# Kernel tuning notes

Measured on AMD Instinct MI355X. Metric: run time of the kernel, lower is better.

The kernel has to match this reference:

```python
import jax, jax.numpy as jnp
import numpy as np
from math import sqrt

CTX_LEN = 24
DK = 92
EMBED_DIM = 36
N_TOKENS = 500
HIDDEN = 152
CONCAT_DIM = 936  # 2*EMBED_DIM + EMBED_DIM*CTX_LEN


def setup_inputs() -> dict:
    key = jax.random.key(0)
    ks = jax.random.split(key, 12)
    u = lambda k, shp, s: jax.random.uniform(k, shp, dtype=jnp.float32) * s
    return {
        "x0": jax.random.normal(ks[0], (EMBED_DIM, CTX_LEN), dtype=jnp.float32),
        "wq1": u(ks[1], (CTX_LEN, DK), 0.05),
        "wk1": u(ks[2], (CTX_LEN, DK), 0.05),
        "wv1": u(ks[3], (CTX_LEN, DK), 0.05),
        "wq2": u(ks[4], (CTX_LEN, DK), 0.05),
        "wk2": u(ks[5], (CTX_LEN, DK), 0.05),
        "wv2": u(ks[6], (CTX_LEN, DK), 0.05),
        "nl0": u(ks[7], (CONCAT_DIM, HIDDEN), 0.05),
        "nl0_bias": u(ks[8], (HIDDEN,), 0.005),
        "nl1": u(ks[9], (HIDDEN, EMBED_DIM), 0.05),
        "ctp": u(ks[10], (EMBED_DIM, N_TOKENS), 0.05),
        "ctp_bias": u(ks[11], (N_TOKENS,), 0.005),
    }


def _self_attn(x, wq, wk, wv):
    # x: (E, C); wq/wk/wv: (C, DK)
    q = x @ wq
    k = x @ wk
    v = x @ wv
    # NOTE: original multiplies by sqrt(dk) (not divide) and softmaxes over dim 0
    scores = jax.nn.softmax((q @ k.T) * sqrt(DK), axis=0)  # (E, E)
    return scores @ v  # (E, DK)


def reference(x0, wq1, wk1, wv1, wq2, wk2, wv2, nl0, nl0_bias, nl1, ctp, ctp_bias):
    t3 = _self_attn(x0, wq1, wk1, wv1).sum(axis=1)   # (E,)
    t13 = _self_attn(x0, wq2, wk2, wv2).sum(axis=1)  # (E,)
    t71 = jnp.concatenate([t3, t13, x0.reshape(-1)])  # (936,)
    t7 = jax.nn.relu(t71 @ nl0) + nl0_bias            # (152,)
    t10 = t7 @ nl1                                    # (E,)
    return t10 @ ctp + ctp_bias                       # (N_TOKENS,)
```

## Files before the change

### kernel.cpp

```cpp
#include <hip/hip_runtime.h>
#include <math.h>

#define CTX 24
#define DKK 92
#define ED 36
#define NTOK 500
#define HID 152

#define NBLK 19
#define COLS 8
#define TOKS 27
#define POISON 0xAAAAAAAAu

typedef float4 f4;

__device__ __forceinline__ float dot4(f4 a, f4 b) {
    return a.x*b.x + a.y*b.y + a.z*b.z + a.w*b.w;
}

struct AttnLds {
    f4    xw4[216];
    f4    W4[144];
    f4    M4[216];
    float S[1296];
    float wvs[24];
    f4    vs24[9];
};

__device__ void attn_wave(int lane, const float* __restrict__ x0,
                          const float* __restrict__ wq, const float* __restrict__ wk,
                          const float* __restrict__ wv,
                          AttnLds& L, float* __restrict__ dst )
{
    const f4* x0g = (const f4*)x0;
    for (int i = lane; i < 216; i += 64) L.xw4[i] = x0g[i];
    if (lane < CTX) {
        const f4* wvr = (const f4*)(wv + lane * DKK);
        f4 s = {0.f, 0.f, 0.f, 0.f};
        #pragma unroll
        for (int c = 0; c < 23; ++c) {
            f4 v = wvr[c];
            s.x += v.x; s.y += v.y; s.z += v.z; s.w += v.w;
        }
        L.wvs[lane] = s.x + s.y + s.z + s.w;
    }
    __threadfence_block();

    {
        const f4* wq4 = (const f4*)wq;
        const f4* wk4 = (const f4*)wk;
        const int a0 = (lane >> 3) * 3, b0 = (lane & 7) * 3;
        float acc[3][3] = {};
        #pragma unroll 4
        for (int dc = 0; dc < 23; ++dc) {
            f4 qa[3], kb[3];
            #pragma unroll
            for (int r = 0; r < 3; ++r) qa[r] = wq4[(a0 + r) * 23 + dc];
            #pragma unroll
            for (int c = 0; c < 3; ++c) kb[c] = wk4[(b0 + c) * 23 + dc];
            #pragma unroll
            for (int r = 0; r < 3; ++r)
                #pragma unroll
                for (int c = 0; c < 3; ++c)
                    acc[r][c] += dot4(qa[r], kb[c]);
        }
        float* Wf = (float*)L.W4;
        #pragma unroll
        for (int r = 0; r < 3; ++r)
            #pragma unroll
            for (int c = 0; c < 3; ++c)
                Wf[(a0 + r) * 24 + b0 + c] = acc[r][c];
    }
    __threadfence_block();

    {
        const float* xf = (const float*)L.xw4;
        for (int t = lane; t < 72; t += 64) {
            const int e0 = (t / 6) * 3, bq = t % 6;
            f4 acc[3] = {};
            #pragma unroll
            for (int a = 0; a < 24; ++a) {
                f4 w = L.W4[a * 6 + bq];
                #pragma unroll
                for (int r = 0; r < 3; ++r) {
                    float x = xf[(e0 + r) * 24 + a];
                    acc[r].x += x * w.x; acc[r].y += x * w.y;
                    acc[r].z += x * w.z; acc[r].w += x * w.w;
                }
            }
            #pragma unroll
            for (int r = 0; r < 3; ++r) L.M4[(e0 + r) * 6 + bq] = acc[r];
        }
    }
    __threadfence_block();

    {
        const float scale = 9.59166304662544f;
        for (int t = lane; t < 108; t += 64) {
            const int e0 = (t / 9) * 3, f0 = (t % 9) * 4;
            float acc[3][4] = {};
            #pragma unroll
            for (int bq = 0; bq < 6; ++bq) {
                f4 m[3], x[4];
                #pragma unroll
                for (int r = 0; r < 3; ++r) m[r] = L.M4[(e0 + r) * 6 + bq];
                #pragma unroll
                for (int c = 0; c < 4; ++c) x[c] = L.xw4[(f0 + c) * 6 + bq];
                #pragma unroll
                for (int r = 0; r < 3; ++r)
                    #pragma unroll
                    for (int c = 0; c < 4; ++c)
                        acc[r][c] += dot4(m[r], x[c]);
            }
            #pragma unroll
            for (int r = 0; r < 3; ++r)
                #pragma unroll
                for (int c = 0; c < 4; ++c)
                    L.S[(e0 + r) * 36 + f0 + c] = acc[r][c] * scale;
        }
    }
    __threadfence_block();

    if (lane < ED) {
        const int f = lane;
        float mx = -1e30f;
        #pragma unroll 4
        for (int e = 0; e < ED; ++e) mx = fmaxf(mx, L.S[e * 36 + f]);
        float sum = 0.f;
        #pragma unroll 4
        for (int e = 0; e < ED; ++e) {
            float p = expf(L.S[e * 36 + f] - mx);
            L.S[e * 36 + f] = p;
            sum += p;
        }
        const float* xf = (const float*)L.xw4;
        float vs = 0.f;
        #pragma unroll
        for (int c = 0; c < CTX; ++c) vs += xf[f * 24 + c] * L.wvs[c];
        ((float*)L.vs24)[f] = vs / sum;
    }
    __threadfence_block();

    if (lane < ED) {
        const int e = lane;
        const f4* Srow = (const f4*)&L.S[e * 36];
        float s = 0.f;
        #pragma unroll
        for (int fq = 0; fq < 9; ++fq) s += dot4(Srow[fq], L.vs24[fq]);
        dst[e] = s;
    }
}

__global__ __launch_bounds__(256) void fused_vpoll(
    const float* __restrict__ x0,
    const float* __restrict__ wq1, const float* __restrict__ wk1, const float* __restrict__ wv1,
    const float* __restrict__ wq2, const float* __restrict__ wk2, const float* __restrict__ wv2,
    const float* __restrict__ nl0, const float* __restrict__ nl0_bias,
    const float* __restrict__ nl1, const float* __restrict__ ctp, const float* __restrict__ ctp_bias,
    float* __restrict__ ws, float* __restrict__ out)
{
    __shared__ AttnLds A0, A1;
    __shared__ float conc72[72];
    __shared__ f4    part4[128][2];
    __shared__ float red[16][COLS];
    __shared__ float corr_red[16][COLS];
    __shared__ float hsAll[HID];
    __shared__ float t10p[144];
    __shared__ float t10s[ED];

    const int b   = blockIdx.x;
    const int tid = threadIdx.x;
    const int c0  = b * COLS;
    unsigned int* h_bits = (unsigned int*)ws;

    if (tid < 64) {
        attn_wave(tid, x0, wq1, wk1, wv1, A0, conc72);
    } else if (tid < 128) {
        attn_wave(tid - 64, x0, wq2, wk2, wv2, A1, conc72 + ED);
    } else {
        const int t2 = tid - 128;
        f4 a0 = {0.f,0.f,0.f,0.f}, a1 = {0.f,0.f,0.f,0.f};
        for (int r = t2; r < 864; r += 128) {
            const float x = x0[r];
            const f4* row = (const f4*)(nl0 + (72 + r) * HID + c0);
            f4 v0 = row[0], v1 = row[1];
            a0.x += x*v0.x; a0.y += x*v0.y; a0.z += x*v0.z; a0.w += x*v0.w;
            a1.x += x*v1.x; a1.y += x*v1.y; a1.z += x*v1.z; a1.w += x*v1.w;
        }
        part4[t2][0] = a0; part4[t2][1] = a1;
    }
    __syncthreads();

    if (tid < 128) {
        const int c = tid & 7, g = tid >> 3;
        const float* pf = (const float*)part4;
        float s = 0.f;
        #pragma unroll
        for (int k = 0; k < 8; ++k) s += pf[(g + 16*k) * 8 + c];
        red[g][c] = s;
    } else {
        const int t3 = tid - 128;
        const int c = t3 & 7, g = t3 >> 3;
        float s = 0.f;
        for (int i = g; i < 72; i += 16)
            s += conc72[i] * nl0[i * HID + c0 + c];
        corr_red[g][c] = s;
    }
    __syncthreads();

    if (tid < COLS) {
        float s = 0.f;
        #pragma unroll
        for (int g = 0; g < 16; ++g) s += red[g][tid] + corr_red[g][tid];
        const float h = fmaxf(s, 0.f) + nl0_bias[c0 + tid];
        __hip_atomic_store(&h_bits[c0 + tid], __float_as_uint(h),
                           __ATOMIC_RELAXED, __HIP_MEMORY_SCOPE_AGENT);
    }

    if (tid < HID) {
        unsigned int v;
        do {
            v = __hip_atomic_load(&h_bits[tid],
                                  __ATOMIC_RELAXED, __HIP_MEMORY_SCOPE_AGENT);
        } while (v == POISON);
        hsAll[tid] = __uint_as_float(v);
    }
    __syncthreads();

    if (tid < 144) {
        const int e = tid % 36, jg = tid / 36;
        float s = 0.f;
        for (int j = jg; j < HID; j += 4) s += hsAll[j] * nl1[j * 36 + e];
        t10p[tid] = s;
    }
    __syncthreads();
    if (tid < ED)
        t10s[tid] = t10p[tid] + t10p[36 + tid] + t10p[72 + tid] + t10p[108 + tid];
    __syncthreads();

    if (tid < TOKS) {
        const int n = b * TOKS + tid;
        if (n < NTOK) {
            float s = ctp_bias[n];
            #pragma unroll
            for (int e = 0; e < ED; ++e) s += t10s[e] * ctp[e * NTOK + n];
            out[n] = s;
        }
    }
}

extern "C" void kernel_launch(void* const* d_in, const int* in_sizes, int n_in,
                              void* d_out, int out_size, void* d_ws, size_t ws_size,
                              hipStream_t stream) {
    const float* x0       = (const float*)d_in[0];
    const float* wq1      = (const float*)d_in[1];
    const float* wk1      = (const float*)d_in[2];
    const float* wv1      = (const float*)d_in[3];
    const float* wq2      = (const float*)d_in[4];
    const float* wk2      = (const float*)d_in[5];
    const float* wv2      = (const float*)d_in[6];
    const float* nl0      = (const float*)d_in[7];
    const float* nl0_bias = (const float*)d_in[8];
    const float* nl1      = (const float*)d_in[9];
    const float* ctp      = (const float*)d_in[10];
    const float* ctp_bias = (const float*)d_in[11];

    fused_vpoll<<<NBLK, 256, 0, stream>>>(x0, wq1, wk1, wv1, wq2, wk2, wv2,
                                          nl0, nl0_bias, nl1, ctp, ctp_bias,
                                          (float*)d_ws, (float*)d_out);
}
```

Baseline: 26.74 us.

## Prefetch nl1, nl0 slices and biases into LDS before the inter-block wait

During the attention phase, the idle waves now stage nl1, the 72-row nl0 correction slice, the nl0 bias and the ctp bias into shared memory, so those global loads overlap compute instead of sitting after the cross-block spin-wait. The poll loop reads four h values per thread across 38 threads instead of one per thread across 152. The final ctp projection is split over 9 partial sums per token, using 243 threads instead of 27, followed by a small reduction. This adds a large LDS footprint (about 22KB more) and an extra barrier.

```diff
diff --git a/kernel.cpp b/kernel.cpp
--- a/kernel.cpp
+++ b/kernel.cpp
@@ -151,7 +151,7 @@
     }
 }
 
-__global__ __launch_bounds__(256) void fused_vpoll(
+__global__ __launch_bounds__(256) void fused_vpoll2(
     const float* __restrict__ x0,
     const float* __restrict__ wq1, const float* __restrict__ wk1, const float* __restrict__ wv1,
     const float* __restrict__ wq2, const float* __restrict__ wk2, const float* __restrict__ wv2,
@@ -164,9 +164,14 @@
     __shared__ f4    part4[128][2];
     __shared__ float red[16][COLS];
     __shared__ float corr_red[16][COLS];
+    __shared__ f4    nl1s4[1368];
+    __shared__ f4    corr72b4[144];
+    __shared__ float nl0b8[COLS];
+    __shared__ float ctpbs[TOKS];
     __shared__ float hsAll[HID];
     __shared__ float t10p[144];
     __shared__ float t10s[ED];
+    __shared__ float tp6[TOKS][9];
 
     const int b   = blockIdx.x;
     const int tid = threadIdx.x;
@@ -188,6 +193,18 @@
             a1.x += x*v1.x; a1.y += x*v1.y; a1.z += x*v1.z; a1.w += x*v1.w;
         }
         part4[t2][0] = a0; part4[t2][1] = a1;
+
+        const f4* nl14 = (const f4*)nl1;
+        for (int q = t2; q < 1368; q += 128) nl1s4[q] = nl14[q];
+        for (int q = t2; q < 144; q += 128) {
+            const int i = q >> 1, half = q & 1;
+            corr72b4[q] = ((const f4*)(nl0 + i * HID + c0))[half];
+        }
+        if (t2 < COLS) nl0b8[t2] = nl0_bias[c0 + t2];
+        if (t2 < TOKS) {
+            const int n = b * TOKS + t2;
+            ctpbs[t2] = (n < NTOK) ? ctp_bias[n] : 0.f;
+        }
     }
     __syncthreads();
 
@@ -201,9 +218,10 @@
     } else {
         const int t3 = tid - 128;
         const int c = t3 & 7, g = t3 >> 3;
+        const float* cb = (const float*)corr72b4;
         float s = 0.f;
         for (int i = g; i < 72; i += 16)
-            s += conc72[i] * nl0[i * HID + c0 + c];
+            s += conc72[i] * cb[i * 8 + c];
         corr_red[g][c] = s;
     }
     __syncthreads();
@@ -212,25 +230,33 @@
         float s = 0.f;
         #pragma unroll
         for (int g = 0; g < 16; ++g) s += red[g][tid] + corr_red[g][tid];
-        const float h = fmaxf(s, 0.f) + nl0_bias[c0 + tid];
+        const float h = fmaxf(s, 0.f) + nl0b8[tid];
         __hip_atomic_store(&h_bits[c0 + tid], __float_as_uint(h),
                            __ATOMIC_RELAXED, __HIP_MEMORY_SCOPE_AGENT);
     }
 
-    if (tid < HID) {
-        unsigned int v;
+    if (tid < 38) {
+        unsigned int w[4];
+        bool ok;
         do {
-            v = __hip_atomic_load(&h_bits[tid],
-                                  __ATOMIC_RELAXED, __HIP_MEMORY_SCOPE_AGENT);
-        } while (v == POISON);
-        hsAll[tid] = __uint_as_float(v);
+            #pragma unroll
+            for (int k = 0; k < 4; ++k)
+                w[k] = __hip_atomic_load(&h_bits[4 * tid + k],
+                                         __ATOMIC_RELAXED, __HIP_MEMORY_SCOPE_AGENT);
+            ok = (w[0] != POISON) && (w[1] != POISON) &&
+                 (w[2] != POISON) && (w[3] != POISON);
+        } while (!ok);
+        #pragma unroll
+        for (int k = 0; k < 4; ++k)
+            hsAll[4 * tid + k] = __uint_as_float(w[k]);
     }
     __syncthreads();
 
     if (tid < 144) {
         const int e = tid % 36, jg = tid / 36;
-        float s = 0.f;
-        for (int j = jg; j < HID; j += 4) s += hsAll[j] * nl1[j * 36 + e];
+        const float* nf = (const float*)nl1s4;
+        float s = 0.f;
+        for (int j = jg; j < HID; j += 4) s += hsAll[j] * nf[j * 36 + e];
         t10p[tid] = s;
     }
     __syncthreads();
@@ -238,12 +264,25 @@
         t10s[tid] = t10p[tid] + t10p[36 + tid] + t10p[72 + tid] + t10p[108 + tid];
     __syncthreads();
 
+    if (tid < TOKS * 9) {
+        const int tok = tid / 9, g = tid % 9;
+        const int n = b * TOKS + tok;
+        if (n < NTOK) {
+            const int e0 = g * 4;
+            float s = t10s[e0]     * ctp[(e0    ) * NTOK + n]
+                    + t10s[e0 + 1] * ctp[(e0 + 1) * NTOK + n]
+                    + t10s[e0 + 2] * ctp[(e0 + 2) * NTOK + n]
+                    + t10s[e0 + 3] * ctp[(e0 + 3) * NTOK + n];
+            tp6[tok][g] = s;
+        }
+    }
+    __syncthreads();
     if (tid < TOKS) {
         const int n = b * TOKS + tid;
         if (n < NTOK) {
-            float s = ctp_bias[n];
-            #pragma unroll
-            for (int e = 0; e < ED; ++e) s += t10s[e] * ctp[e * NTOK + n];
+            float s = ctpbs[tid];
+            #pragma unroll
+            for (int g = 0; g < 9; ++g) s += tp6[tid][g];
             out[n] = s;
         }
     }
@@ -265,7 +304,7 @@
     const float* ctp      = (const float*)d_in[10];
     const float* ctp_bias = (const float*)d_in[11];
 
-    fused_vpoll<<<NBLK, 256, 0, stream>>>(x0, wq1, wk1, wv1, wq2, wk2, wv2,
-                                          nl0, nl0_bias, nl1, ctp, ctp_bias,
-                                          (float*)d_ws, (float*)d_out);
+    fused_vpoll2<<<NBLK, 256, 0, stream>>>(x0, wq1, wk1, wv1, wq2, wk2, wv2,
+                                           nl0, nl0_bias, nl1, ctp, ctp_bias,
+                                           (float*)d_ws, (float*)d_out);
 }
```

Result: faster. 24.48 us (-8.4%).
